# Optimization experiments

Hardware: AMD Instinct MI355X
Metric: run time of the kernel (lower is better)

The kernel has to match this reference:

```python
import jax, jax.numpy as jnp
import numpy as np

WINDOW_SIZE = 128
NEG = -1e9

def setup_inputs() -> dict:
    key = jax.random.key(0)
    kq, kk, kv = jax.random.split(key, 3)
    B, H, T, D = 2, 16, 2048, 64
    q = jax.random.normal(kq, (B, H, T, D), dtype=jnp.float32)
    k = jax.random.normal(kk, (B, H, T, D), dtype=jnp.float32)
    v = jax.random.normal(kv, (B, H, T, D), dtype=jnp.float32)
    return {"q": q, "k": k, "v": v}

def reference(q, k, v):
    # q,k,v: (B, H, T, D)
    D = q.shape[-1]
    Tq, Tk = q.shape[2], k.shape[2]
    scale = 1.0 / jnp.sqrt(jnp.asarray(D, dtype=q.dtype))
    scores = jnp.einsum('bhqd,bhkd->bhqk', q, k) * scale  # (B,H,Tq,Tk)
    dist = jnp.abs(jnp.arange(Tq)[:, None] - jnp.arange(Tk)[None, :])
    window_mask = dist <= WINDOW_SIZE  # (Tq,Tk)
    scores = jnp.where(window_mask[None, None], scores, jnp.asarray(NEG, dtype=scores.dtype))
    attn = jax.nn.softmax(scores, axis=-1)
    output = jnp.einsum('bhqk,bhkd->bhqd', attn, v)
    return (output, attn)
```

## Files before the change

### kernel.cpp

```cpp
#include <hip/hip_runtime.h>
#include <hip/hip_bf16.h>

typedef short bf16x8 __attribute__((ext_vector_type(8)));
typedef short bf16x4 __attribute__((ext_vector_type(4)));
typedef float f32x4 __attribute__((ext_vector_type(4)));

#define T_DIM 2048
#define D_DIM 64
#define WIN 128
#define QBLK 64
#define NKT_MAX 20
#define ACCT 17
#define NEGBIG -1e30f

__device__ __forceinline__ short f2b(float x) {
  __hip_bfloat16 h = __float2bfloat16(x);
  return *reinterpret_cast<short*>(&h);
}
__device__ __forceinline__ float b2f(short s) {
  unsigned u = ((unsigned)(unsigned short)s) << 16;
  return __builtin_bit_cast(float, u);
}
__device__ __forceinline__ bf16x8 cvt8(f32x4 a, f32x4 b) {
  bf16x8 r;
  r[0] = f2b(a[0]); r[1] = f2b(a[1]); r[2] = f2b(a[2]); r[3] = f2b(a[3]);
  r[4] = f2b(b[0]); r[5] = f2b(b[1]); r[6] = f2b(b[2]); r[7] = f2b(b[3]);
  return r;
}
__device__ __forceinline__ int swz(int row, int b) { return row * 640 + (b ^ ((row & 7) << 4)); }

__global__ __launch_bounds__(256, 2) void lsa_one(
    const float* __restrict__ Qg, const float* __restrict__ Kg,
    const float* __restrict__ Vg, float* __restrict__ Og,
    float* __restrict__ Ag) {
  const int tid = threadIdx.x;
  const int work = ((blockIdx.x & 7) << 7) + (blockIdx.x >> 3);
  const int bh = work >> 5;
  const int q0 = (work & 31) * QBLK;
  int kstart = q0 - WIN; if (kstart < 0) kstart = 0;
  int kend = q0 + QBLK + WIN; if (kend > T_DIM) kend = T_DIM;
  const int KW = kend - kstart;
  const int nkt = KW >> 4;

  const float* qptr = Qg + (size_t)bh * (T_DIM * D_DIM);
  const float* kptr = Kg + (size_t)bh * (T_DIM * D_DIM);
  const float* vptr = Vg + (size_t)bh * (T_DIM * D_DIM);
  float* optr = Og + (size_t)bh * (T_DIM * D_DIM);
  float* aptr = Ag + (size_t)bh * ((size_t)T_DIM * T_DIM);

  __shared__ __align__(16) char Vb[D_DIM * 640];
  __shared__ __align__(16) char Pb[QBLK * 640];

  for (int idx = tid; idx < KW * 16; idx += 256) {
    const int r = idx >> 4, c4 = idx & 15;
    f32x4 f = *(const f32x4*)(vptr + (size_t)(kstart + r) * D_DIM + c4 * 4);
    const int d0 = c4 * 4;
    *(short*)(Vb + swz(d0 + 0, r * 2)) = f2b(f[0]);
    *(short*)(Vb + swz(d0 + 1, r * 2)) = f2b(f[1]);
    *(short*)(Vb + swz(d0 + 2, r * 2)) = f2b(f[2]);
    *(short*)(Vb + swz(d0 + 3, r * 2)) = f2b(f[3]);
  }
  __syncthreads();

  const int lane = tid & 63, w = tid >> 6, c = lane & 15, hi = lane >> 4;

  const float* qrow = qptr + (size_t)(q0 + w * 16 + c) * D_DIM + 8 * hi;
  const bf16x8 a0 = cvt8(*(const f32x4*)qrow, *(const f32x4*)(qrow + 4));
  const bf16x8 a1 = cvt8(*(const f32x4*)(qrow + 32), *(const f32x4*)(qrow + 36));

  int klo = q0 + w * 16 - WIN - kstart; if (klo < 0) klo = 0;
  const int kt0 = klo >> 4;
  int kt1 = (q0 + w * 16 + 15 + WIN + 1 - kstart + 15) >> 4; if (kt1 > nkt) kt1 = nkt;
  const int s0 = kt0 >> 1, s1 = (kt1 + 1) >> 1;
  const int nlive = kt1 - kt0;

  f32x4 acc[ACCT];
#pragma unroll
  for (int i = 0; i < ACCT; ++i) {
    acc[i] = (f32x4){0.f, 0.f, 0.f, 0.f};
    if (i < nlive) {
      const float* kr = kptr + (size_t)(kstart + (kt0 + i) * 16 + c) * D_DIM + 8 * hi;
      const bf16x8 b0 = cvt8(*(const f32x4*)kr, *(const f32x4*)(kr + 4));
      const bf16x8 b1 = cvt8(*(const f32x4*)(kr + 32), *(const f32x4*)(kr + 36));
      acc[i] = __builtin_amdgcn_mfma_f32_16x16x32_bf16(a0, b0, acc[i], 0, 0, 0);
      acc[i] = __builtin_amdgcn_mfma_f32_16x16x32_bf16(a1, b1, acc[i], 0, 0, 0);
    }
  }

  const int kgc = kstart + c;
#pragma unroll
  for (int j = 0; j < 4; ++j) {
    const int qr = q0 + w * 16 + 4 * hi + j;
    const int prow = w * 16 + 4 * hi + j;
    float m = NEGBIG;
#pragma unroll
    for (int i = 0; i < ACCT; ++i)
      if (i < nlive) {
        float s = acc[i][j] * 0.125f;
        const int kcol = kgc + (kt0 + i) * 16;
        int dist = qr - kcol; dist = dist < 0 ? -dist : dist;
        s = (dist <= WIN) ? s : NEGBIG;
        acc[i][j] = s;
        m = fmaxf(m, s);
      }
    m = fmaxf(m, __shfl_xor(m, 1));
    m = fmaxf(m, __shfl_xor(m, 2));
    m = fmaxf(m, __shfl_xor(m, 4));
    m = fmaxf(m, __shfl_xor(m, 8));
    float sum = 0.f;
#pragma unroll
    for (int i = 0; i < ACCT; ++i)
      if (i < nlive) {
        const float p = __expf(acc[i][j] - m);
        acc[i][j] = p;
        sum += p;
      }
    sum += __shfl_xor(sum, 1);
    sum += __shfl_xor(sum, 2);
    sum += __shfl_xor(sum, 4);
    sum += __shfl_xor(sum, 8);
    const float inv = 1.f / sum;
#pragma unroll
    for (int i = 0; i < ACCT; ++i)
      if (i < nlive)
        *(short*)(Pb + swz(prow, ((kt0 + i) * 16 + c) * 2)) = f2b(acc[i][j] * inv);
    for (int t = 0; t < kt0; ++t)
      *(short*)(Pb + swz(prow, (t * 16 + c) * 2)) = 0;
    for (int t = kt1; t < nkt; ++t)
      *(short*)(Pb + swz(prow, (t * 16 + c) * 2)) = 0;
  }

  for (int rr = 0; rr < 16; ++rr) {
    const int r = w * 16 + rr;
    float* dst = aptr + (size_t)(q0 + r) * T_DIM;
#pragma unroll
    for (int i = 0; i < 8; ++i) {
      const int col = i * 256 + lane * 4;
      f32x4 val = {0.f, 0.f, 0.f, 0.f};
      if (col >= kstart && col < kend) {
        const bf16x4 pv = *(const bf16x4*)(Pb + swz(r, (col - kstart) * 2));
        val[0] = b2f(pv[0]); val[1] = b2f(pv[1]); val[2] = b2f(pv[2]); val[3] = b2f(pv[3]);
      }
      __builtin_nontemporal_store(val, (f32x4*)(dst + col));
    }
  }

  f32x4 ov[4];
#pragma unroll
  for (int dt = 0; dt < 4; ++dt) ov[dt] = (f32x4){0.f, 0.f, 0.f, 0.f};
  for (int s = s0; s < s1; ++s) {
    const bf16x8 pa = *(const bf16x8*)(Pb + swz(w * 16 + c, 64 * s + 16 * hi));
#pragma unroll
    for (int dt = 0; dt < 4; ++dt) {
      const bf16x8 vb = *(const bf16x8*)(Vb + swz(dt * 16 + c, 64 * s + 16 * hi));
      ov[dt] = __builtin_amdgcn_mfma_f32_16x16x32_bf16(pa, vb, ov[dt], 0, 0, 0);
    }
  }
#pragma unroll
  for (int dt = 0; dt < 4; ++dt)
#pragma unroll
    for (int j = 0; j < 4; ++j)
      __builtin_nontemporal_store(
          ov[dt][j], optr + (size_t)(q0 + w * 16 + 4 * hi + j) * D_DIM + dt * 16 + c);
}

extern "C" void kernel_launch(void* const* d_in, const int* in_sizes, int n_in,
                              void* d_out, int out_size, void* d_ws, size_t ws_size,
                              hipStream_t stream) {
  const float* q = (const float*)d_in[0];
  const float* k = (const float*)d_in[1];
  const float* v = (const float*)d_in[2];
  float* out = (float*)d_out;
  float* attn = out + (size_t)2 * 16 * T_DIM * D_DIM;
  lsa_one<<<dim3(2 * 16 * (T_DIM / QBLK)), dim3(256), 0, stream>>>(q, k, v, out, attn);
}
```

Baseline: 134.3 us.

## Transpose QK^T MFMA so each lane owns a query row; vectorize P stores

Swaps the MFMA operands so the score tile is laid out with queries along lanes, which turns the per-row softmax reductions into two cross-lane shuffles instead of four per row and lets probabilities be written to LDS as packed 4-element bf16 stores. The V-staging barrier is moved to after the attention-matrix write so V loading overlaps the QK and softmax work. Risk: the attention-row write loop reads Pb rows written only by the same wave, which is fine, but the barrier move relies on that invariant.

```diff
diff --git a/kernel.cpp b/kernel.cpp
--- a/kernel.cpp
+++ b/kernel.cpp
@@ -9,7 +9,6 @@
 #define D_DIM 64
 #define WIN 128
 #define QBLK 64
-#define NKT_MAX 20
 #define ACCT 17
 #define NEGBIG -1e30f
 
@@ -60,13 +59,12 @@
     *(short*)(Vb + swz(d0 + 2, r * 2)) = f2b(f[2]);
     *(short*)(Vb + swz(d0 + 3, r * 2)) = f2b(f[3]);
   }
-  __syncthreads();
 
   const int lane = tid & 63, w = tid >> 6, c = lane & 15, hi = lane >> 4;
 
   const float* qrow = qptr + (size_t)(q0 + w * 16 + c) * D_DIM + 8 * hi;
-  const bf16x8 a0 = cvt8(*(const f32x4*)qrow, *(const f32x4*)(qrow + 4));
-  const bf16x8 a1 = cvt8(*(const f32x4*)(qrow + 32), *(const f32x4*)(qrow + 36));
+  const bf16x8 qb0 = cvt8(*(const f32x4*)qrow, *(const f32x4*)(qrow + 4));
+  const bf16x8 qb1 = cvt8(*(const f32x4*)(qrow + 32), *(const f32x4*)(qrow + 36));
 
   int klo = q0 + w * 16 - WIN - kstart; if (klo < 0) klo = 0;
   const int kt0 = klo >> 4;
@@ -82,52 +80,57 @@
       const float* kr = kptr + (size_t)(kstart + (kt0 + i) * 16 + c) * D_DIM + 8 * hi;
       const bf16x8 b0 = cvt8(*(const f32x4*)kr, *(const f32x4*)(kr + 4));
       const bf16x8 b1 = cvt8(*(const f32x4*)(kr + 32), *(const f32x4*)(kr + 36));
-      acc[i] = __builtin_amdgcn_mfma_f32_16x16x32_bf16(a0, b0, acc[i], 0, 0, 0);
-      acc[i] = __builtin_amdgcn_mfma_f32_16x16x32_bf16(a1, b1, acc[i], 0, 0, 0);
+      acc[i] = __builtin_amdgcn_mfma_f32_16x16x32_bf16(b0, qb0, acc[i], 0, 0, 0);
+      acc[i] = __builtin_amdgcn_mfma_f32_16x16x32_bf16(b1, qb1, acc[i], 0, 0, 0);
     }
   }
 
-  const int kgc = kstart + c;
+  const int qr = q0 + w * 16 + c;
+  const int kb = kstart + 4 * hi;
+  float m = NEGBIG;
 #pragma unroll
-  for (int j = 0; j < 4; ++j) {
-    const int qr = q0 + w * 16 + 4 * hi + j;
-    const int prow = w * 16 + 4 * hi + j;
-    float m = NEGBIG;
+  for (int i = 0; i < ACCT; ++i)
+    if (i < nlive) {
 #pragma unroll
-    for (int i = 0; i < ACCT; ++i)
-      if (i < nlive) {
+      for (int j = 0; j < 4; ++j) {
         float s = acc[i][j] * 0.125f;
-        const int kcol = kgc + (kt0 + i) * 16;
+        const int kcol = kb + (kt0 + i) * 16 + j;
         int dist = qr - kcol; dist = dist < 0 ? -dist : dist;
         s = (dist <= WIN) ? s : NEGBIG;
         acc[i][j] = s;
         m = fmaxf(m, s);
       }
-    m = fmaxf(m, __shfl_xor(m, 1));
-    m = fmaxf(m, __shfl_xor(m, 2));
-    m = fmaxf(m, __shfl_xor(m, 4));
-    m = fmaxf(m, __shfl_xor(m, 8));
-    float sum = 0.f;
+    }
+  m = fmaxf(m, __shfl_xor(m, 16));
+  m = fmaxf(m, __shfl_xor(m, 32));
+  float sum = 0.f;
 #pragma unroll
-    for (int i = 0; i < ACCT; ++i)
-      if (i < nlive) {
+  for (int i = 0; i < ACCT; ++i)
+    if (i < nlive) {
+#pragma unroll
+      for (int j = 0; j < 4; ++j) {
         const float p = __expf(acc[i][j] - m);
         acc[i][j] = p;
         sum += p;
       }
-    sum += __shfl_xor(sum, 1);
-    sum += __shfl_xor(sum, 2);
-    sum += __shfl_xor(sum, 4);
-    sum += __shfl_xor(sum, 8);
-    const float inv = 1.f / sum;
+    }
+  sum += __shfl_xor(sum, 16);
+  sum += __shfl_xor(sum, 32);
+  const float inv = 1.f / sum;
+
+  const int prow = w * 16 + c;
 #pragma unroll
-    for (int i = 0; i < ACCT; ++i)
-      if (i < nlive)
-        *(short*)(Pb + swz(prow, ((kt0 + i) * 16 + c) * 2)) = f2b(acc[i][j] * inv);
-    for (int t = 0; t < kt0; ++t)
-      *(short*)(Pb + swz(prow, (t * 16 + c) * 2)) = 0;
-    for (int t = kt1; t < nkt; ++t)
-      *(short*)(Pb + swz(prow, (t * 16 + c) * 2)) = 0;
+  for (int i = 0; i < ACCT; ++i)
+    if (i < nlive) {
+      bf16x4 pk;
+#pragma unroll
+      for (int j = 0; j < 4; ++j) pk[j] = f2b(acc[i][j] * inv);
+      *(bf16x4*)(Pb + swz(prow, 32 * (kt0 + i) + 8 * hi)) = pk;
+    }
+  {
+    const bf16x4 z4 = {0, 0, 0, 0};
+    for (int t = 0; t < kt0; ++t) *(bf16x4*)(Pb + swz(prow, 32 * t + 8 * hi)) = z4;
+    for (int t = kt1; t < nkt; ++t) *(bf16x4*)(Pb + swz(prow, 32 * t + 8 * hi)) = z4;
   }
 
   for (int rr = 0; rr < 16; ++rr) {
@@ -144,6 +147,8 @@
       __builtin_nontemporal_store(val, (f32x4*)(dst + col));
     }
   }
+
+  __syncthreads();
 
   f32x4 ov[4];
 #pragma unroll
```

Result: faster. 129.0 us (-4.0%).
